# Performance work log

Hardware: AMD Instinct MI355X
Metric: run time of the kernel (lower is better)

The kernel has to match this reference:

```python
import jax, jax.numpy as jnp
import numpy as np
import math


def setup_inputs() -> dict:
    key = jax.random.key(0)
    ks = jax.random.split(key, 10)
    B, N, C, heads = 16, 1024, 256, 8
    nW = 4
    ANGLE_BINS = 5
    inner = C  # dim_head*heads == dim
    return {
        "x": jax.random.normal(ks[0], (B, N, C), jnp.float32),
        "mask": jax.random.normal(ks[1], (nW, N, N), jnp.float32),
        "affine_matrix": jax.random.normal(ks[2], (B, 2, 3), jnp.float32),
        "Wq": jax.random.normal(ks[3], (C, inner), jnp.float32) * (C ** -0.5),
        "bq": jnp.zeros((inner,), jnp.float32),
        "Wkv": jax.random.normal(ks[4], (C, 2 * inner), jnp.float32) * (C ** -0.5),
        "bkv": jnp.zeros((2 * inner,), jnp.float32),
        "Wp": jax.random.normal(ks[5], (C, C), jnp.float32) * (C ** -0.5),
        "bp": jnp.zeros((C,), jnp.float32),
        "angle_table": jnp.ones((ANGLE_BINS, heads), jnp.float32),
        "H": 32,
        "W": 32,
    }


def reference(x, mask, affine_matrix, Wq, bq, Wkv, bkv, Wp, bp, angle_table, H, W):
    B, N, C = x.shape
    heads = angle_table.shape[1]
    hd = C // heads
    scale = hd ** -0.5

    # qkv projections (torch Linear -> x @ W + b with W stored as (in, out))
    q = (x @ Wq + bq).reshape(B, N, heads, hd).transpose(0, 2, 1, 3)      # (B,h,N,d)
    kv = (x @ Wkv + bkv).reshape(B, N, 2, heads, hd).transpose(2, 0, 3, 1, 4)
    k, v = kv[0], kv[1]                                                    # (B,h,N,d)

    attn = jnp.einsum('bhqd,bhkd->bhqk', q * scale, k)                     # (B,h,N,N)

    # angle bias: per-query multiplicative bias in (1,2)
    grid_y, grid_x = jnp.meshgrid(jnp.arange(H), jnp.arange(W), indexing='ij')
    coords = jnp.stack([grid_x.reshape(-1), grid_y.reshape(-1)], -1).astype(jnp.float32)  # (N,2)
    center = jnp.array([W / 2.0, H / 2.0], jnp.float32)
    ego = jnp.einsum('bij,j->bi', affine_matrix[:, :2, :2], center) + affine_matrix[:, :2, 2]  # (B,2)
    rel = coords[None, :, :] - ego[:, None, :]                             # (B,N,2)
    ang = jnp.arctan2(rel[..., 1], rel[..., 0])
    bins = (((ang + math.pi) / (2.0 * math.pi)) * (angle_table.shape[0] - 1)).astype(jnp.int32)
    bias = 1.0 + jax.nn.sigmoid(angle_table[bins])                         # (B,N,h)
    attn = attn * bias.transpose(0, 2, 1)[..., None]                       # broadcast over keys

    # additive window mask then softmax
    nW = mask.shape[0]
    attn = attn.reshape(B // nW, nW, heads, N, N) + mask[None, :, None]
    attn = jax.nn.softmax(attn.reshape(B, heads, N, N), axis=-1)

    out = jnp.einsum('bhqk,bhkd->bhqd', attn, v).transpose(0, 2, 1, 3).reshape(B, N, C)
    return out @ Wp + bp
```

## Files before the change

### kernel.cpp

```cpp
#include <hip/hip_runtime.h>
#include <hip/hip_bf16.h>
#include <math.h>

#define BB 16
#define NTOK 1024
#define CDIM 256
#define HEADS 8
#define HD 32
#define LOG2E 1.4426950408889634f
#define PSHIFT 18.0f

typedef __attribute__((ext_vector_type(8))) _Float16 half8;
typedef __attribute__((ext_vector_type(8))) unsigned short u16x8;
typedef __attribute__((ext_vector_type(4))) unsigned int u32x4;
typedef __attribute__((ext_vector_type(4))) float f32x4;

__device__ __forceinline__ unsigned short f2h(float f) {
  _Float16 h = (_Float16)f;
  return __builtin_bit_cast(unsigned short, h);
}
__device__ __forceinline__ half8 ldh8(const unsigned short* p) {
  return *reinterpret_cast<const half8*>(p);
}
__device__ __forceinline__ void gl_lds16(const unsigned short* g,
                                         unsigned short* l) {
  __builtin_amdgcn_global_load_lds(
      (const __attribute__((address_space(1))) unsigned int*)g,
      (__attribute__((address_space(3))) unsigned int*)l, 16, 0, 0);
}

__global__ __launch_bounds__(256) void cvt_x(const float* __restrict__ X,
                                             unsigned short* __restrict__ x16) {
  size_t base = ((size_t)blockIdx.x * 256 + threadIdx.x) * 8;
  float4 a = *(const float4*)(X + base);
  float4 b = *(const float4*)(X + base + 4);
  u16x8 o = {f2h(a.x), f2h(a.y), f2h(a.z), f2h(a.w),
             f2h(b.x), f2h(b.y), f2h(b.z), f2h(b.w)};
  *(u16x8*)(x16 + base) = o;
}

__global__ __launch_bounds__(256) void cvt_w(
    const float* __restrict__ Wq, const float* __restrict__ Wkv,
    const float* __restrict__ Wp, unsigned short* __restrict__ wt16,
    unsigned short* __restrict__ wp16) {
  int idx = blockIdx.x * 256 + threadIdx.x;
  float val; size_t dst; bool isp = false;
  if (idx < 65536) {
    int k = idx >> 8, n = idx & 255;
    val = Wq[idx]; dst = (size_t)n * 256 + k;
  } else if (idx < 196608) {
    int i2 = idx - 65536;
    int k = i2 >> 9, n2 = i2 & 511;
    val = Wkv[i2]; dst = (size_t)(256 + n2) * 256 + k;
  } else {
    int i3 = idx - 196608;
    int k = i3 >> 8, n = i3 & 255;
    val = Wp[i3]; dst = (size_t)n * 256 + k; isp = true;
  }
  unsigned short h = f2h(val);
  if (isp) wp16[dst] = h; else wt16[dst] = h;
}

__global__ __launch_bounds__(256) void bias_kernel(
    const float* __restrict__ affine, const float* __restrict__ atab,
    float* __restrict__ bias) {
  int idx = blockIdx.x * 256 + threadIdx.x;
  if (idx >= BB * NTOK) return;
  int b = idx >> 10, n = idx & (NTOK - 1);
  float cx = (float)(n & 31);
  float cy = (float)(n >> 5);
  const float* A = affine + b * 6;
  float egx = fmaf(A[0], 16.f, fmaf(A[1], 16.f, A[2]));
  float egy = fmaf(A[3], 16.f, fmaf(A[4], 16.f, A[5]));
  float ang = atan2f(cy - egy, cx - egx);
  float t = (ang + 3.14159265358979323846f) *
            (1.f / (2.f * 3.14159265358979323846f)) * 4.f;
  int bin = (int)t;
  bin = bin < 0 ? 0 : (bin > 4 ? 4 : bin);
  for (int h = 0; h < HEADS; ++h) {
    float a = atab[bin * HEADS + h];
    float s = 1.f / (1.f + __expf(-a));
    bias[((size_t)b * HEADS + h) * NTOK + n] = 1.f + s;
  }
}

__global__ __launch_bounds__(256) void mask_prepF(const float* __restrict__ m,
                                                  float* __restrict__ mF) {
  int idx = blockIdx.x * 256 + threadIdx.x;
  int b4 = idx >> 18;
  int rem = idx & 262143;
  int q = rem >> 8;
  int k = (rem & 255) * 4;
  float4 v = *(const float4*)(m + ((size_t)b4 * NTOK + q) * NTOK + k);
  float4 o = {fmaf(v.x, LOG2E, -PSHIFT), fmaf(v.y, LOG2E, -PSHIFT),
              fmaf(v.z, LOG2E, -PSHIFT), fmaf(v.w, LOG2E, -PSHIFT)};
  int kt = k >> 5;
  int m0 = (k & 31) >> 1;
  size_t base = ((size_t)(b4 * 64 + kt * 2)) * 16384 + q * 16 + m0;
  float2 e = {o.x, o.z};
  float2 d = {o.y, o.w};
  *(float2*)(mF + base) = e;
  *(float2*)(mF + base + 16384) = d;
}

__global__ __launch_bounds__(512, 4) void gemm_qkv16(
    const unsigned short* __restrict__ x16, const unsigned short* __restrict__ wt16,
    const float* __restrict__ bq, const float* __restrict__ bkv,
    const float* __restrict__ bias, unsigned short* __restrict__ q16,
    unsigned short* __restrict__ k16, unsigned short* __restrict__ vt16) {
  __shared__ __align__(16) unsigned short SM[16384];
  unsigned short* Xs = SM;
  unsigned short* Ws = SM + 8192;
  int tid = threadIdx.x;
  int w = tid >> 6, l = tid & 63;
  int row16 = l & 15, grp = l >> 4;
  int bid = blockIdx.x;
  int xcd = bid & 7, local = bid >> 3;
  int jb = local % 6, mb = xcd * 16 + local / 6;
  int j0 = jb * 128, m0 = mb * 128;
  int wm = w >> 1, wn = w & 1;

  auto stg = [&](int nb, int kt) {
    int k0s = kt * 32;
    int row = w * 16 + (l >> 2);
    int ge = (((l & 3) * 16) ^ ((row & 3) << 4)) >> 1;
    gl_lds16(x16 + (size_t)(m0 + row) * 256 + k0s + ge, Xs + nb * 4096 + w * 512);
    gl_lds16(wt16 + (size_t)(j0 + row) * 256 + k0s + ge, Ws + nb * 4096 + w * 512);
  };
  auto off16 = [&](int row, int g) {
    return row * 32 + ((((g * 16) ^ ((row & 3) << 4))) >> 1);
  };

  stg(0, 0);
  __syncthreads();

  f32x4 acc[2][4];
#pragma unroll
  for (int i = 0; i < 2; ++i)
#pragma unroll
    for (int c = 0; c < 4; ++c) acc[i][c] = (f32x4){0.f, 0.f, 0.f, 0.f};

  for (int kt = 0; kt < 8; ++kt) {
    int cur = kt & 1;
    if (kt < 7) stg(cur ^ 1, kt + 1);
    half8 a0 = ldh8(Xs + cur * 4096 + off16(wm * 32 + row16, grp));
    half8 a1 = ldh8(Xs + cur * 4096 + off16(wm * 32 + 16 + row16, grp));
#pragma unroll
    for (int c = 0; c < 4; ++c) {
      half8 bh = ldh8(Ws + cur * 4096 + off16(wn * 64 + c * 16 + row16, grp));
      acc[0][c] = __builtin_amdgcn_mfma_f32_16x16x32_f16(a0, bh, acc[0][c], 0, 0, 0);
      acc[1][c] = __builtin_amdgcn_mfma_f32_16x16x32_f16(a1, bh, acc[1][c], 0, 0, 0);
    }
    __syncthreads();
  }

  const float scaleq = 0.17677669529663687f * LOG2E;
  int half_mine = wm >> 1;
  for (int half = 0; half < 2; ++half) {
    if (half_mine == half) {
#pragma unroll
      for (int i = 0; i < 2; ++i) {
#pragma unroll
        for (int c = 0; c < 4; ++c) {
          int col = wn * 64 + c * 16 + row16;
          int jg = j0 + col;
#pragma unroll
          for (int r = 0; r < 4; ++r) {
            int rowl = (wm & 1) * 32 + i * 16 + grp * 4 + r;
            int m = m0 + half * 64 + rowl;
            int b = m >> 10, n = m & (NTOK - 1);
            float val = acc[i][c][r];
            unsigned short o;
            if (jb < 2)
              o = f2h((val + bq[jg]) * scaleq *
                      bias[((size_t)b * HEADS + (jg >> 5)) * NTOK + n]);
            else
              o = f2h(val + bkv[jg - CDIM]);
            SM[rowl * 136 + col] = o;
          }
        }
      }
    }
    __syncthreads();
    if (jb < 4) {
#pragma unroll
      for (int it = 0; it < 2; ++it) {
        int lin = it * 512 + tid;
        int rowb = lin >> 4, oct = lin & 15;
        u16x8 v = *(const u16x8*)&SM[rowb * 136 + oct * 8];
        int m = m0 + half * 64 + rowb;
        int b = m >> 10, n = m & (NTOK - 1);
        int jg = j0 + oct * 8;
        unsigned short* dst; int h, d;
        if (jb < 2) { h = jg >> 5; d = jg & 31; dst = q16; }
        else { int c2 = jg - CDIM; h = c2 >> 5; d = c2 & 31; dst = k16; }
        *(u16x8*)(dst + (((size_t)b * HEADS + h) * NTOK + n) * HD + d) = v;
      }
    } else {
#pragma unroll
      for (int it = 0; it < 2; ++it) {
        int lin = it * 512 + tid;
        int noct = lin >> 7, jl = lin & 127;
        u16x8 v;
#pragma unroll
        for (int e = 0; e < 8; ++e) v[e] = SM[(noct * 8 + e) * 136 + jl];
        int c3 = j0 + jl - 2 * CDIM;
        int h = c3 >> 5, d = c3 & 31;
        int n0 = m0 + half * 64 + noct * 8;
        int b = n0 >> 10, nn = n0 & (NTOK - 1);
        *(u16x8*)(vt16 + (((size_t)b * HEADS + h) * HD + d) * NTOK + nn) = v;
      }
    }
    __syncthreads();
  }
}

__global__ __launch_bounds__(512, 4) void attn16(
    const unsigned short* __restrict__ q16, const unsigned short* __restrict__ k16,
    const unsigned short* __restrict__ vt16, const float* __restrict__ maskF,
    unsigned short* __restrict__ ao16) {
  __shared__ __align__(16) unsigned short KT[2][4][1024];
  __shared__ __align__(16) unsigned short VT[2][4][1024];

  int tid = threadIdx.x;
  int w = tid >> 6, l = tid & 63;
  int row16 = l & 15, grp = l >> 4;
  int bid = blockIdx.x;
  int g = (bid >> 6) * 8 + (bid & 7);
  int inner = (bid >> 3) & 7;
  int qt = g >> 2, b4 = g & 3;
  int brep = inner >> 1, hg = inner & 1;
  int b = brep * 4 + b4;
  int hl = w >> 1, qh = w & 1;
  int head = hg * 4 + hl;
  int bh = b * HEADS + head;
  int qbase = qt * 64 + qh * 32;

  half8 bq[2];
#pragma unroll
  for (int qb = 0; qb < 2; ++qb)
    bq[qb] = ldh8(q16 + ((size_t)bh * NTOK + qbase + qb * 16 + row16) * HD +
                  grp * 8);

  const float* mFb = maskF + (size_t)b4 * 64 * 16384;

  f32x4 acc[2][2];
#pragma unroll
  for (int i = 0; i < 2; ++i)
#pragma unroll
    for (int j = 0; j < 2; ++j) acc[i][j] = (f32x4){0.f, 0.f, 0.f, 0.f};
  float lsum[2] = {0.f, 0.f};

  auto off32 = [&](int row, int gg) {
    return row * 32 + ((gg ^ ((row >> 1) & 3)) << 3);
  };

  auto stage = [&](int nb, int kt2) {
    int k0n = (kt2 & 31) * 32;
    int key = 2 * (l >> 2) + qh;
    int sk = (l & 3) ^ ((qh * 8 + (l >> 3)) & 3);
    gl_lds16(k16 + ((size_t)bh * NTOK + k0n + key) * HD + sk * 8,
             &KT[nb][hl][qh * 512]);
    int dl = qh * 16 + (l >> 2);
    int sv = (l & 3) ^ ((qh * 8 + (l >> 3)) & 3);
    gl_lds16(vt16 + ((size_t)bh * HD + dl) * NTOK + k0n + sv * 8,
             &VT[nb][hl][qh * 512]);
  };

  stage(0, 0);
  __syncthreads();

  for (int kt = 0; kt < 32; ++kt) {
    int cur = kt & 1;
    if (kt < 31) stage(cur ^ 1, kt + 1);

    half8 kf0 = ldh8(&KT[cur][hl][off32(row16, grp)]);
    half8 kf1 = ldh8(&KT[cur][hl][off32(16 + row16, grp)]);
    half8 v0 = ldh8(&VT[cur][hl][off32(row16, grp)]);
    half8 v1 = ldh8(&VT[cur][hl][off32(16 + row16, grp)]);

#pragma unroll
    for (int qb = 0; qb < 2; ++qb) {
      const float* mp = mFb + (size_t)(kt * 2) * 16384 +
                        (qbase + qb * 16 + row16) * 16 + grp * 4;
      f32x4 mC0 = *(const f32x4*)mp;
      f32x4 mC1 = *(const f32x4*)(mp + 16384);
      f32x4 s0 = __builtin_amdgcn_mfma_f32_16x16x32_f16(kf0, bq[qb], mC0, 0, 0, 0);
      f32x4 s1 = __builtin_amdgcn_mfma_f32_16x16x32_f16(kf1, bq[qb], mC1, 0, 0, 0);
      f32x4 e0, e1;
#pragma unroll
      for (int r = 0; r < 4; ++r) {
        e0[r] = __builtin_amdgcn_exp2f(s0[r]);
        e1[r] = __builtin_amdgcn_exp2f(s1[r]);
      }
      lsum[qb] += ((e0[0] + e1[0]) + (e0[1] + e1[1])) +
                  ((e0[2] + e1[2]) + (e0[3] + e1[3]));
      u32x4 pk;
#pragma unroll
      for (int r = 0; r < 4; ++r)
        pk[r] = __builtin_bit_cast(unsigned,
                                   __builtin_amdgcn_cvt_pkrtz(e0[r], e1[r]));
      half8 pa = __builtin_bit_cast(half8, pk);
      acc[qb][0] = __builtin_amdgcn_mfma_f32_16x16x32_f16(pa, v0, acc[qb][0], 0, 0, 0);
      acc[qb][1] = __builtin_amdgcn_mfma_f32_16x16x32_f16(pa, v1, acc[qb][1], 0, 0, 0);
    }
    __syncthreads();
  }

#pragma unroll
  for (int qb = 0; qb < 2; ++qb) {
    lsum[qb] += __shfl_xor(lsum[qb], 16);
    lsum[qb] += __shfl_xor(lsum[qb], 32);
  }
#pragma unroll
  for (int qb = 0; qb < 2; ++qb) {
#pragma unroll
    for (int r = 0; r < 4; ++r) {
      float lr = __shfl(lsum[qb], grp * 4 + r, 16);
      float inv = 1.f / lr;
      int qrow = qbase + qb * 16 + grp * 4 + r;
      size_t obase = ((size_t)b * NTOK + qrow) * CDIM + head * HD;
      ao16[obase + row16] = f2h(acc[qb][0][r] * inv);
      ao16[obase + 16 + row16] = f2h(acc[qb][1][r] * inv);
    }
  }
}

__global__ __launch_bounds__(512, 4) void gemm_out16(
    const unsigned short* __restrict__ a16, const unsigned short* __restrict__ wp16,
    const float* __restrict__ bp, float* __restrict__ out) {
  __shared__ __align__(16) unsigned short SM[16384];
  unsigned short* Xs = SM;
  unsigned short* Ws = SM + 8192;
  int tid = threadIdx.x;
  int w = tid >> 6, l = tid & 63;
  int row16 = l & 15, grp = l >> 4;
  int bid = blockIdx.x;
  int xcd = bid & 7, local = bid >> 3;
  int jb = local & 1, mb = xcd * 16 + (local >> 1);
  int j0 = jb * 128, m0 = mb * 128;
  int wm = w >> 1, wn = w & 1;

  auto stg = [&](int nb, int kt) {
    int k0s = kt * 32;
    int row = w * 16 + (l >> 2);
    int ge = (((l & 3) * 16) ^ ((row & 3) << 4)) >> 1;
    gl_lds16(a16 + (size_t)(m0 + row) * 256 + k0s + ge, Xs + nb * 4096 + w * 512);
    gl_lds16(wp16 + (size_t)(j0 + row) * 256 + k0s + ge, Ws + nb * 4096 + w * 512);
  };
  auto off16 = [&](int row, int g) {
    return row * 32 + ((((g * 16) ^ ((row & 3) << 4))) >> 1);
  };

  stg(0, 0);
  __syncthreads();

  f32x4 acc[2][4];
#pragma unroll
  for (int i = 0; i < 2; ++i)
#pragma unroll
    for (int c = 0; c < 4; ++c) acc[i][c] = (f32x4){0.f, 0.f, 0.f, 0.f};

  for (int kt = 0; kt < 8; ++kt) {
    int cur = kt & 1;
    if (kt < 7) stg(cur ^ 1, kt + 1);
    half8 a0 = ldh8(Xs + cur * 4096 + off16(wm * 32 + row16, grp));
    half8 a1 = ldh8(Xs + cur * 4096 + off16(wm * 32 + 16 + row16, grp));
#pragma unroll
    for (int c = 0; c < 4; ++c) {
      half8 bh = ldh8(Ws + cur * 4096 + off16(wn * 64 + c * 16 + row16, grp));
      acc[0][c] = __builtin_amdgcn_mfma_f32_16x16x32_f16(a0, bh, acc[0][c], 0, 0, 0);
      acc[1][c] = __builtin_amdgcn_mfma_f32_16x16x32_f16(a1, bh, acc[1][c], 0, 0, 0);
    }
    __syncthreads();
  }

#pragma unroll
  for (int i = 0; i < 2; ++i) {
    int ng = m0 + wm * 32 + i * 16 + grp * 4;
#pragma unroll
    for (int c = 0; c < 4; ++c) {
      int jg = j0 + wn * 64 + c * 16 + row16;
      float bias = bp[jg];
#pragma unroll
      for (int r = 0; r < 4; ++r) {
        out[(size_t)(ng + r) * CDIM + jg] = acc[i][c][r] + bias;
      }
    }
  }
}

extern "C" void kernel_launch(void* const* d_in, const int* in_sizes, int n_in,
                              void* d_out, int out_size, void* d_ws,
                              size_t ws_size, hipStream_t stream) {
  const float* x = (const float*)d_in[0];
  const float* mask = (const float*)d_in[1];
  const float* affine = (const float*)d_in[2];
  const float* Wq = (const float*)d_in[3];
  const float* bq = (const float*)d_in[4];
  const float* Wkv = (const float*)d_in[5];
  const float* bkv = (const float*)d_in[6];
  const float* Wp = (const float*)d_in[7];
  const float* bp = (const float*)d_in[8];
  const float* atab = (const float*)d_in[9];
  float* out = (float*)d_out;

  const size_t bhnd = (size_t)BB * HEADS * NTOK * HD;
  unsigned short* q16 = (unsigned short*)d_ws;
  unsigned short* k16 = q16 + bhnd;
  unsigned short* vt16 = k16 + bhnd;
  unsigned short* x16 = vt16 + bhnd;
  unsigned short* wt16 = x16 + bhnd;
  unsigned short* wp16 = wt16 + 768 * 256;
  float* bias = (float*)(wp16 + 256 * 256);
  float* maskF = bias + (size_t)BB * HEADS * NTOK;

  cvt_x<<<2048, 256, 0, stream>>>(x, x16);
  cvt_w<<<1024, 256, 0, stream>>>(Wq, Wkv, Wp, wt16, wp16);
  bias_kernel<<<64, 256, 0, stream>>>(affine, atab, bias);
  mask_prepF<<<4096, 256, 0, stream>>>(mask, maskF);
  gemm_qkv16<<<768, 512, 0, stream>>>(x16, wt16, bq, bkv, bias, q16, k16, vt16);
  attn16<<<512, 512, 0, stream>>>(q16, k16, vt16, maskF, x16);
  gemm_out16<<<256, 512, 0, stream>>>(x16, wp16, bp, out);
}
```

Before: 95.96 us.

## Fuse mask preprocessing into attention kernel via LDS-staged raw mask tiles

Removes the separate mask_prepF kernel, which read the 16 MB fp32 mask and wrote a reordered, prescaled copy. The attention kernel now streams raw mask tiles into a double-buffered, swizzled LDS region alongside K and V using global_load_lds. The log2e scaling and shift move into per-element FMAs after the QK MFMA. This saves a full mask read/write pass and a launch, at the cost of extra LDS, extra ALU work in the inner loop, and the mask no longer being folded into the MFMA accumulator.

New measurement: 89.87 us. 1.07x faster.

```diff
diff --git a/kernel.cpp b/kernel.cpp
--- a/kernel.cpp
+++ b/kernel.cpp
@@ -22,8 +22,7 @@
 __device__ __forceinline__ half8 ldh8(const unsigned short* p) {
   return *reinterpret_cast<const half8*>(p);
 }
-__device__ __forceinline__ void gl_lds16(const unsigned short* g,
-                                         unsigned short* l) {
+__device__ __forceinline__ void gl_lds16(const void* g, void* l) {
   __builtin_amdgcn_global_load_lds(
       (const __attribute__((address_space(1))) unsigned int*)g,
       (__attribute__((address_space(3))) unsigned int*)l, 16, 0, 0);
@@ -84,25 +83,6 @@
   }
 }
 
-__global__ __launch_bounds__(256) void mask_prepF(const float* __restrict__ m,
-                                                  float* __restrict__ mF) {
-  int idx = blockIdx.x * 256 + threadIdx.x;
-  int b4 = idx >> 18;
-  int rem = idx & 262143;
-  int q = rem >> 8;
-  int k = (rem & 255) * 4;
-  float4 v = *(const float4*)(m + ((size_t)b4 * NTOK + q) * NTOK + k);
-  float4 o = {fmaf(v.x, LOG2E, -PSHIFT), fmaf(v.y, LOG2E, -PSHIFT),
-              fmaf(v.z, LOG2E, -PSHIFT), fmaf(v.w, LOG2E, -PSHIFT)};
-  int kt = k >> 5;
-  int m0 = (k & 31) >> 1;
-  size_t base = ((size_t)(b4 * 64 + kt * 2)) * 16384 + q * 16 + m0;
-  float2 e = {o.x, o.z};
-  float2 d = {o.y, o.w};
-  *(float2*)(mF + base) = e;
-  *(float2*)(mF + base + 16384) = d;
-}
-
 __global__ __launch_bounds__(512, 4) void gemm_qkv16(
     const unsigned short* __restrict__ x16, const unsigned short* __restrict__ wt16,
     const float* __restrict__ bq, const float* __restrict__ bkv,
@@ -217,10 +197,11 @@
 
 __global__ __launch_bounds__(512, 4) void attn16(
     const unsigned short* __restrict__ q16, const unsigned short* __restrict__ k16,
-    const unsigned short* __restrict__ vt16, const float* __restrict__ maskF,
+    const unsigned short* __restrict__ vt16, const float* __restrict__ mask,
     unsigned short* __restrict__ ao16) {
   __shared__ __align__(16) unsigned short KT[2][4][1024];
   __shared__ __align__(16) unsigned short VT[2][4][1024];
+  __shared__ __align__(16) float MT[2][2048];
 
   int tid = threadIdx.x;
   int w = tid >> 6, l = tid & 63;
@@ -234,7 +215,8 @@
   int hl = w >> 1, qh = w & 1;
   int head = hg * 4 + hl;
   int bh = b * HEADS + head;
-  int qbase = qt * 64 + qh * 32;
+  int q0g = qt * 64;
+  int qbase = q0g + qh * 32;
 
   half8 bq[2];
 #pragma unroll
@@ -242,7 +224,7 @@
     bq[qb] = ldh8(q16 + ((size_t)bh * NTOK + qbase + qb * 16 + row16) * HD +
                   grp * 8);
 
-  const float* mFb = maskF + (size_t)b4 * 64 * 16384;
+  const float* mbase = mask + (size_t)b4 * NTOK * NTOK;
 
   f32x4 acc[2][2];
 #pragma unroll
@@ -250,6 +232,7 @@
 #pragma unroll
     for (int j = 0; j < 2; ++j) acc[i][j] = (f32x4){0.f, 0.f, 0.f, 0.f};
   float lsum[2] = {0.f, 0.f};
+  const f32x4 c18 = (f32x4){-PSHIFT, -PSHIFT, -PSHIFT, -PSHIFT};
 
   auto off32 = [&](int row, int gg) {
     return row * 32 + ((gg ^ ((row >> 1) & 3)) << 3);
@@ -265,6 +248,10 @@
     int sv = (l & 3) ^ ((qh * 8 + (l >> 3)) & 3);
     gl_lds16(vt16 + ((size_t)bh * HD + dl) * NTOK + k0n + sv * 8,
              &VT[nb][hl][qh * 512]);
+    int qq = w * 8 + (l >> 3);
+    int slot = (l & 7) ^ (qq & 7);
+    gl_lds16(mbase + (size_t)(q0g + qq) * NTOK + k0n + slot * 4,
+             &MT[nb][w * 256]);
   };
 
   stage(0, 0);
@@ -281,18 +268,21 @@
 
 #pragma unroll
     for (int qb = 0; qb < 2; ++qb) {
-      const float* mp = mFb + (size_t)(kt * 2) * 16384 +
-                        (qbase + qb * 16 + row16) * 16 + grp * 4;
-      f32x4 mC0 = *(const f32x4*)mp;
-      f32x4 mC1 = *(const f32x4*)(mp + 16384);
-      f32x4 s0 = __builtin_amdgcn_mfma_f32_16x16x32_f16(kf0, bq[qb], mC0, 0, 0, 0);
-      f32x4 s1 = __builtin_amdgcn_mfma_f32_16x16x32_f16(kf1, bq[qb], mC1, 0, 0, 0);
+      int qr = qh * 32 + qb * 16 + row16;
+      int q7 = qr & 7;
+      f32x4 mv0 = *(const f32x4*)&MT[cur][cur * 0 + qr * 32 + (((2 * grp) ^ q7) << 2)];
+      f32x4 mv1 = *(const f32x4*)&MT[cur][qr * 32 + (((2 * grp + 1) ^ q7) << 2)];
+      f32x4 s0 = __builtin_amdgcn_mfma_f32_16x16x32_f16(kf0, bq[qb], c18, 0, 0, 0);
+      f32x4 s1 = __builtin_amdgcn_mfma_f32_16x16x32_f16(kf1, bq[qb], c18, 0, 0, 0);
       f32x4 e0, e1;
-#pragma unroll
-      for (int r = 0; r < 4; ++r) {
-        e0[r] = __builtin_amdgcn_exp2f(s0[r]);
-        e1[r] = __builtin_amdgcn_exp2f(s1[r]);
-      }
+      e0[0] = __builtin_amdgcn_exp2f(fmaf(mv0[0], LOG2E, s0[0]));
+      e1[0] = __builtin_amdgcn_exp2f(fmaf(mv0[1], LOG2E, s1[0]));
+      e0[1] = __builtin_amdgcn_exp2f(fmaf(mv0[2], LOG2E, s0[1]));
+      e1[1] = __builtin_amdgcn_exp2f(fmaf(mv0[3], LOG2E, s1[1]));
+      e0[2] = __builtin_amdgcn_exp2f(fmaf(mv1[0], LOG2E, s0[2]));
+      e1[2] = __builtin_amdgcn_exp2f(fmaf(mv1[1], LOG2E, s1[2]));
+      e0[3] = __builtin_amdgcn_exp2f(fmaf(mv1[2], LOG2E, s0[3]));
+      e1[3] = __builtin_amdgcn_exp2f(fmaf(mv1[3], LOG2E, s1[3]));
       lsum[qb] += ((e0[0] + e1[0]) + (e0[1] + e1[1])) +
                   ((e0[2] + e1[2]) + (e0[3] + e1[3]));
       u32x4 pk;
@@ -413,13 +403,11 @@
   unsigned short* wt16 = x16 + bhnd;
   unsigned short* wp16 = wt16 + 768 * 256;
   float* bias = (float*)(wp16 + 256 * 256);
-  float* maskF = bias + (size_t)BB * HEADS * NTOK;
 
   cvt_x<<<2048, 256, 0, stream>>>(x, x16);
   cvt_w<<<1024, 256, 0, stream>>>(Wq, Wkv, Wp, wt16, wp16);
   bias_kernel<<<64, 256, 0, stream>>>(affine, atab, bias);
-  mask_prepF<<<4096, 256, 0, stream>>>(mask, maskF);
   gemm_qkv16<<<768, 512, 0, stream>>>(x16, wt16, bq, bkv, bias, q16, k16, vt16);
-  attn16<<<512, 512, 0, stream>>>(q16, k16, vt16, maskF, x16);
+  attn16<<<512, 512, 0, stream>>>(q16, k16, vt16, mask, x16);
   gemm_out16<<<256, 512, 0, stream>>>(x16, wp16, bp, out);
 }
```
